# Optimization experiments

Hardware: AMD Instinct MI355X
Metric: run time of the kernel (lower is better)

The kernel has to match this reference:

```python
import jax, jax.numpy as jnp
import numpy as np

LEAF = 32
N = 262144          # num_nodes, power of 2
NLEV = 8            # HODLR levels
RANK = 16           # off-diagonal low-rank
NNZ = 1310720       # ~5 nnz per row


def setup_inputs() -> dict:
    key = jax.random.key(0)
    ks = jax.random.split(key, 24)
    inp = {}
    inp["leaf_blocks"] = jax.random.normal(ks[0], (1, N // LEAF, LEAF, LEAF), jnp.float32) * 0.1
    for l in range(NLEV):
        inp[f"u{l}"] = jax.random.normal(ks[1 + 2 * l], (1, N, RANK), jnp.float32) * 0.05
        inp[f"v{l}"] = jax.random.normal(ks[2 + 2 * l], (1, N, RANK), jnp.float32) * 0.05
    inp["A_indices"] = jax.random.randint(ks[17], (2, NNZ), 0, N, dtype=jnp.int32).astype(jnp.int64)
    inp["A_values"] = jax.random.normal(ks[18], (NNZ,), jnp.float32)
    inp["z"] = jax.random.normal(ks[19], (1, N, 1), jnp.float32)
    inp["num_nodes"] = N
    return inp


def apply_hodlr(leaf_blocks, factors, x, leaf_size=LEAF):
    # x: [B, n, 1]; leaf_blocks: [B, n/leaf, leaf, leaf]
    B, n, _ = x.shape
    nb = n // leaf_size
    xb = x.reshape(B, nb, leaf_size, 1)
    L = leaf_blocks
    # y = L @ (L^T @ x) + 1e-4 * x  per leaf block
    yb = jnp.matmul(L, jnp.matmul(jnp.swapaxes(L, -1, -2), xb)) + xb * 1e-4
    y = yb.reshape(B, n, 1)
    for li, (u, v) in enumerate(factors):
        num_splits = 2 ** (li + 1)
        bs = n // num_splits
        if bs == 0:
            continue
        npair = num_splits // 2
        vl = npair * 2 * bs  # == n for power-of-2 n
        xv = x[:, :vl].reshape(B, npair, 2, bs, 1)
        uv = u[:, :vl].reshape(B, npair, 2, bs, -1)
        vv = v[:, :vl].reshape(B, npair, 2, bs, -1)
        xL, xR = xv[:, :, 0], xv[:, :, 1]
        uL, uR = uv[:, :, 0], uv[:, :, 1]
        vL, vR = vv[:, :, 0], vv[:, :, 1]
        # cross-block low-rank updates: y_L += U_L (V_R^T x_R), y_R += U_R (V_L^T x_L)
        yL = jnp.matmul(uL, jnp.matmul(jnp.swapaxes(vR, -1, -2), xR))
        yR = jnp.matmul(uR, jnp.matmul(jnp.swapaxes(vL, -1, -2), xL))
        upd = jnp.stack([yL, yR], axis=2).reshape(B, vl, 1)
        if vl < n:
            upd = jnp.pad(upd, ((0, 0), (0, n - vl), (0, 0)))
        y = y + upd
    return y


def reference(leaf_blocks, u0, v0, u1, v1, u2, v2, u3, v3, u4, v4, u5, v5, u6, v6, u7, v7,
              A_indices, A_values, z, num_nodes):
    factors = [(u0, v0), (u1, v1), (u2, v2), (u3, v3),
               (u4, v4), (u5, v5), (u6, v6), (u7, v7)]
    w = apply_hodlr(leaf_blocks, factors, z)           # [1, N, 1]
    w_flat = w[0, :, 0]                                 # [N]
    rows, cols = A_indices[0], A_indices[1]
    # sparse COO matvec: y[r] = sum_k A_values[k] * w[cols[k]] over rows
    y_flat = jax.ops.segment_sum(A_values * w_flat[cols], rows, num_segments=num_nodes)
    y = y_flat.reshape(1, num_nodes, 1)
    return jnp.mean((y - z) ** 2)
```

## Files before the change

kernel.cpp:

```cpp
#include <hip/hip_runtime.h>

#define NN 262144
#define RANK 16
#define NNZ_K 1310720
#define NB 512
#define BPB 2560
#define NBKT 256
#define RPB 1024
#define NCH 2048

struct P8 { const float* p[8]; };

__global__ __launch_bounds__(256, 6) void k_levels_t(P8 v, const float* __restrict__ z,
                                                     float* __restrict__ part) {
    __shared__ float red[8][4][16];
    const int tid  = threadIdx.x;
    const int base = blockIdx.x * 128;
    const int q    = tid & 3;
    const int e    = tid >> 2;
    const int lane = tid & 63;
    const int wv   = tid >> 6;

#pragma unroll
    for (int g = 0; g < 2; ++g) {
        float4 acc[4];
#pragma unroll
        for (int l = 0; l < 4; ++l) acc[l] = make_float4(0.f, 0.f, 0.f, 0.f);

#pragma unroll
        for (int it = 0; it < 2; ++it) {
            const int jl = it * 64 + e;
            const size_t j = (size_t)(base + jl);
            const float zz = z[j];
            float4 vv[4];
#pragma unroll
            for (int l = 0; l < 4; ++l)
                vv[l] = *(const float4*)(v.p[g * 4 + l] + j * RANK + q * 4);
#pragma unroll
            for (int l = 0; l < 4; ++l) {
                acc[l].x += vv[l].x * zz;
                acc[l].y += vv[l].y * zz;
                acc[l].z += vv[l].z * zz;
                acc[l].w += vv[l].w * zz;
            }
        }

#pragma unroll
        for (int l = 0; l < 4; ++l) {
            float4 a = acc[l];
#pragma unroll
            for (int m = 4; m <= 32; m <<= 1) {
                a.x += __shfl_xor(a.x, m);
                a.y += __shfl_xor(a.y, m);
                a.z += __shfl_xor(a.z, m);
                a.w += __shfl_xor(a.w, m);
            }
            if (lane < 4) *(float4*)&red[g * 4 + l][wv][lane * 4] = a;
        }
    }
    __syncthreads();

    if (tid < 128) {
        const int l = tid >> 4;
        const int r = tid & 15;
        const float s = red[l][0][r] + red[l][1][r] + red[l][2][r] + red[l][3][r];
        part[(l * NCH + blockIdx.x) * 16 + r] = s;
    }
}

__global__ __launch_bounds__(256) void k_reduce_t(const float* __restrict__ part,
                                                  float* __restrict__ tg,
                                                  float* __restrict__ loss) {
    const int b = blockIdx.x;
    if (b == 0 && threadIdx.x == 0) loss[0] = 0.f;
    const int t = b + 2;
    const int l = 30 - __clz(t);
    const int h = t - (2 << l);
    const int cnt = 1024 >> l;
    const int c0  = h * cnt;
    const int r = threadIdx.x & 15;
    const int g = threadIdx.x >> 4;

    float s = 0.f;
    for (int c = c0 + g; c < c0 + cnt; c += 16)
        s += part[(l * NCH + c) * 16 + r];

    __shared__ float red[256];
    red[threadIdx.x] = s;
    __syncthreads();
    if (threadIdx.x < 16) {
        float ss = 0.f;
#pragma unroll
        for (int k = 0; k < 16; ++k) ss += red[k * 16 + r];
        tg[((2 << l) - 2 + h) * 16 + r] = ss;
    }
}

__global__ __launch_bounds__(256, 6) void k_w(const float* __restrict__ leaf, P8 u,
                                              const float* __restrict__ z,
                                              const float* __restrict__ tg,
                                              float* __restrict__ w,
                                              float* __restrict__ y) {
    __shared__ float wl[128];
    __shared__ float pb[128];
    __shared__ float tl[8][16];

    const int tid  = threadIdx.x;
    const int base = blockIdx.x * 128;

    if (tid < 128) {
        const int l = tid >> 4;
        const int r = tid & 15;
        const int h = base >> (17 - l);
        tl[l][r] = tg[(((2 << l) - 2) + (h ^ 1)) * 16 + r];
    }

    {
        const int l6 = tid & 63;
        const int wv = tid >> 6;
        const int b  = blockIdx.x * 4 + wv;
        const int r  = l6 >> 1;

        const float* Lb = leaf + (size_t)b * 1024 + r * 32 + (l6 & 1) * 16;
        const float4 L0 = ((const float4*)Lb)[0];
        const float4 L1 = ((const float4*)Lb)[1];
        const float4 L2 = ((const float4*)Lb)[2];
        const float4 L3 = ((const float4*)Lb)[3];

        const float zl = z[b * 32 + (l6 & 31)];
        const float xr = __shfl(zl, r);

        float4 t0 = make_float4(L0.x * xr, L0.y * xr, L0.z * xr, L0.w * xr);
        float4 t1 = make_float4(L1.x * xr, L1.y * xr, L1.z * xr, L1.w * xr);
        float4 t2 = make_float4(L2.x * xr, L2.y * xr, L2.z * xr, L2.w * xr);
        float4 t3 = make_float4(L3.x * xr, L3.y * xr, L3.z * xr, L3.w * xr);

#pragma unroll
        for (int m = 2; m <= 32; m <<= 1) {
            t0.x += __shfl_xor(t0.x, m); t0.y += __shfl_xor(t0.y, m);
            t0.z += __shfl_xor(t0.z, m); t0.w += __shfl_xor(t0.w, m);
            t1.x += __shfl_xor(t1.x, m); t1.y += __shfl_xor(t1.y, m);
            t1.z += __shfl_xor(t1.z, m); t1.w += __shfl_xor(t1.w, m);
            t2.x += __shfl_xor(t2.x, m); t2.y += __shfl_xor(t2.y, m);
            t2.z += __shfl_xor(t2.z, m); t2.w += __shfl_xor(t2.w, m);
            t3.x += __shfl_xor(t3.x, m); t3.y += __shfl_xor(t3.y, m);
            t3.z += __shfl_xor(t3.z, m); t3.w += __shfl_xor(t3.w, m);
        }

        float yp = L0.x * t0.x + L0.y * t0.y + L0.z * t0.z + L0.w * t0.w
                 + L1.x * t1.x + L1.y * t1.y + L1.z * t1.z + L1.w * t1.w
                 + L2.x * t2.x + L2.y * t2.y + L2.z * t2.z + L2.w * t2.w
                 + L3.x * t3.x + L3.y * t3.y + L3.z * t3.z + L3.w * t3.w;
        yp += __shfl_xor(yp, 1);

        const float w0  = yp + 1e-4f * xr;
        const float out = __shfl(w0, (l6 & 31) * 2);
        if (l6 < 32) wl[wv * 32 + l6] = out;
    }
    __syncthreads();

    const int half = tid >> 7;
    const int e    = tid & 127;
    const size_t i = (size_t)(base + e);
    const int l0   = half * 4;

    float accs[4];
#pragma unroll
    for (int lp = 0; lp < 2; ++lp) {
        const int l = l0 + lp * 2;
        float4 a[8];
        {
            const float4* up0 = (const float4*)(u.p[l] + i * RANK);
            const float4* up1 = (const float4*)(u.p[l + 1] + i * RANK);
#pragma unroll
            for (int k = 0; k < 4; ++k) a[k]     = up0[k];
#pragma unroll
            for (int k = 0; k < 4; ++k) a[4 + k] = up1[k];
        }
#pragma unroll
        for (int s = 0; s < 2; ++s) {
            const float4 t0 = *(const float4*)&tl[l + s][0];
            const float4 t1 = *(const float4*)&tl[l + s][4];
            const float4 t2 = *(const float4*)&tl[l + s][8];
            const float4 t3 = *(const float4*)&tl[l + s][12];
            const float4* av = &a[s * 4];
            accs[lp * 2 + s] = av[0].x * t0.x + av[0].y * t0.y + av[0].z * t0.z + av[0].w * t0.w
                             + av[1].x * t1.x + av[1].y * t1.y + av[1].z * t1.z + av[1].w * t1.w
                             + av[2].x * t2.x + av[2].y * t2.y + av[2].z * t2.z + av[2].w * t2.w
                             + av[3].x * t3.x + av[3].y * t3.y + av[3].z * t3.z + av[3].w * t3.w;
        }
    }
    const float sum = (accs[0] + accs[1]) + (accs[2] + accs[3]);
    if (half) pb[e] = sum;
    __syncthreads();
    if (!half) {
        w[i] = wl[e] + sum + pb[e];
        if (y) y[i] = 0.f;
    }
}

__global__ __launch_bounds__(640) void k_bin(const int* __restrict__ idx,
                                             const float* __restrict__ vals,
                                             const float* __restrict__ w,
                                             unsigned long long* __restrict__ gpairs,
                                             int* __restrict__ gdesc) {
    __shared__ unsigned long long pairs[BPB];
    __shared__ int hist[NBKT];
    __shared__ int scan[NBKT];
    __shared__ int cursor[NBKT];

    const int t  = threadIdx.x;
    const int bl = blockIdx.x;
    const int base = bl * BPB;

    if (t < NBKT) hist[t] = 0;
    __syncthreads();

    int   rows[4];
    float pv[4];
    {
        const int k = base + t * 4;
        const int4   r4 = *(const int4*)(idx + k);
        const int4   c4 = *(const int4*)(idx + NNZ_K + k);
        const float4 v4 = *(const float4*)(vals + k);
        rows[0] = r4.x; pv[0] = v4.x * w[c4.x];
        rows[1] = r4.y; pv[1] = v4.y * w[c4.y];
        rows[2] = r4.z; pv[2] = v4.z * w[c4.z];
        rows[3] = r4.w; pv[3] = v4.w * w[c4.w];
        atomicAdd(&hist[r4.x >> 10], 1);
        atomicAdd(&hist[r4.y >> 10], 1);
        atomicAdd(&hist[r4.z >> 10], 1);
        atomicAdd(&hist[r4.w >> 10], 1);
    }
    __syncthreads();

    int cnt = 0;
    if (t < NBKT) { cnt = hist[t]; scan[t] = cnt; }
    __syncthreads();
    for (int off = 1; off < NBKT; off <<= 1) {
        int add = 0;
        if (t >= off && t < NBKT) add = scan[t - off];
        __syncthreads();
        if (t < NBKT) scan[t] += add;
        __syncthreads();
    }
    if (t < NBKT) {
        const int st = scan[t] - cnt;
        gdesc[t * NB + bl] = st | (cnt << 16);
        cursor[t] = st;
    }
    __syncthreads();

#pragma unroll
    for (int i = 0; i < 4; ++i) {
        const int b   = rows[i] >> 10;
        const int pos = atomicAdd(&cursor[b], 1);
        pairs[pos] = ((unsigned long long)__float_as_uint(pv[i]) << 32) | (unsigned)rows[i];
    }
    __syncthreads();

    const ulonglong2* ps = (const ulonglong2*)pairs;
    ulonglong2*       pd = (ulonglong2*)(gpairs + (size_t)bl * BPB);
#pragma unroll
    for (int i = 0; i < 2; ++i)
        pd[i * 640 + t] = ps[i * 640 + t];
}

__global__ __launch_bounds__(1024) void k_accum(const unsigned long long* __restrict__ gpairs,
                                                const int* __restrict__ gdesc,
                                                const float* __restrict__ z,
                                                float* __restrict__ loss) {
    __shared__ float acc[RPB];
    __shared__ float red[16];
    const int t = threadIdx.x;
    const int b = blockIdx.x;
    acc[t] = 0.f;
    __syncthreads();

    {
        const int s  = t >> 1;
        const int h  = t & 1;
        const int d  = gdesc[b * NB + s];
        const int st = d & 0xffff;
        const int c  = d >> 16;
        const unsigned long long* p = gpairs + (size_t)s * BPB + st;
        for (int j = h; j < c; j += 2) {
            const unsigned long long pr = p[j];
            atomicAdd(&acc[(int)(pr & 1023u)], __uint_as_float((unsigned)(pr >> 32)));
        }
    }
    __syncthreads();

    const float d = acc[t] - z[b * RPB + t];
    float s = d * d;
#pragma unroll
    for (int m = 32; m >= 1; m >>= 1) s += __shfl_down(s, m);
    if ((t & 63) == 0) red[t >> 6] = s;
    __syncthreads();
    if (t == 0) {
        float tt = 0.f;
#pragma unroll
        for (int i = 0; i < 16; ++i) tt += red[i];
        atomicAdd(loss, tt);
    }
}

__global__ __launch_bounds__(256) void k_spmv(const int* __restrict__ idx,
                                              const float* __restrict__ vals,
                                              const float* __restrict__ w,
                                              float* __restrict__ y) {
    const int k = (blockIdx.x * 256 + threadIdx.x) * 4;
    const int4   r4 = *(const int4*)(idx + k);
    const int4   c4 = *(const int4*)(idx + NNZ_K + k);
    const float4 v4 = *(const float4*)(vals + k);
    atomicAdd(&y[r4.x], v4.x * w[c4.x]);
    atomicAdd(&y[r4.y], v4.y * w[c4.y]);
    atomicAdd(&y[r4.z], v4.z * w[c4.z]);
    atomicAdd(&y[r4.w], v4.w * w[c4.w]);
}

__global__ __launch_bounds__(256) void k_loss(const float* __restrict__ y,
                                              const float* __restrict__ z,
                                              float* __restrict__ loss) {
    const int i = blockIdx.x * 256 + threadIdx.x;
    const float4 a = ((const float4*)y)[i];
    const float4 b = ((const float4*)z)[i];
    const float dx = a.x - b.x, dy = a.y - b.y, dz = a.z - b.z, dw = a.w - b.w;
    float s = dx * dx + dy * dy + dz * dz + dw * dw;
#pragma unroll
    for (int m = 32; m >= 1; m >>= 1) s += __shfl_down(s, m);
    __shared__ float r4s[4];
    const int lane = threadIdx.x & 63, wv = threadIdx.x >> 6;
    if (lane == 0) r4s[wv] = s;
    __syncthreads();
    if (threadIdx.x == 0) atomicAdd(loss, r4s[0] + r4s[1] + r4s[2] + r4s[3]);
}

__global__ void k_fin(const float* __restrict__ loss, float* __restrict__ out) {
    out[0] = loss[0] * (1.0f / (float)NN);
}

extern "C" void kernel_launch(void* const* d_in, const int* in_sizes, int n_in,
                              void* d_out, int out_size, void* d_ws, size_t ws_size,
                              hipStream_t stream) {
    const float* leaf = (const float*)d_in[0];
    P8 u, v;
    for (int l = 0; l < 8; ++l) {
        u.p[l] = (const float*)d_in[1 + 2 * l];
        v.p[l] = (const float*)d_in[2 + 2 * l];
    }
    const int*   Aidx  = (const int*)d_in[17];
    const float* Avals = (const float*)d_in[18];
    const float* z     = (const float*)d_in[19];

    float* ws   = (float*)d_ws;
    float* part  = ws;
    float* tg    = ws + 262144;
    float* loss  = ws + 270336;
    float* w     = ws + 270400;
    int*   gdesc = (int*)(ws + 532544);
    unsigned long long* gpairs = (unsigned long long*)(ws + 663616);
    const size_t need_main = (size_t)(663616 + (size_t)NB * BPB * 2) * 4;

    k_levels_t<<<NCH, 256, 0, stream>>>(v, z, part);
    k_reduce_t<<<510, 256, 0, stream>>>(part, tg, loss);

    if (ws_size >= need_main) {
        k_w    <<<NN / 128, 256, 0, stream>>>(leaf, u, z, tg, w, nullptr);
        k_bin  <<<NB, 640, 0, stream>>>(Aidx, Avals, w, gpairs, gdesc);
        k_accum<<<NBKT, 1024, 0, stream>>>(gpairs, gdesc, z, loss);
    } else {
        float* y = ws + 532544;
        k_w    <<<NN / 128, 256, 0, stream>>>(leaf, u, z, tg, w, y);
        k_spmv <<<NNZ_K / 1024, 256, 0, stream>>>(Aidx, Avals, w, y);
        k_loss <<<NN / 1024, 256, 0, stream>>>(y, z, loss);
    }
    k_fin<<<1, 1, 0, stream>>>(loss, (float*)d_out);
}
```

Baseline: 355.0 us.

## Fuse leaf-block apply with V-projection pass and fold final loss into accumulator

Merges the V^T z projection and the leaf-block diagonal apply into one heterogeneous kernel, so the two independent phases run concurrently instead of in separate launches. The U-update becomes its own lighter kernel that adds onto the leaf result already stored in w. The projection now covers 256 rows per block, which halves the partial buffer and the reduction work. The final-loss kernel is replaced by a last-block-done counter in k_accum, which removes a launch but adds an atomic fence and an extra read-modify-write of w.

New measurement: 349.8 us. Within noise of the previous version (-1.5%).

```diff
diff --git a/kernel.cpp b/kernel.cpp
--- a/kernel.cpp
+++ b/kernel.cpp
@@ -7,118 +7,68 @@
 #define BPB 2560
 #define NBKT 256
 #define RPB 1024
-#define NCH 2048
+#define SPAN 256
+#define NSP 1024
 
 struct P8 { const float* p[8]; };
 
-__global__ __launch_bounds__(256, 6) void k_levels_t(P8 v, const float* __restrict__ z,
-                                                     float* __restrict__ part) {
-    __shared__ float red[8][4][16];
-    const int tid  = threadIdx.x;
-    const int base = blockIdx.x * 128;
-    const int q    = tid & 3;
-    const int e    = tid >> 2;
-    const int lane = tid & 63;
-    const int wv   = tid >> 6;
-
-#pragma unroll
-    for (int g = 0; g < 2; ++g) {
-        float4 acc[4];
-#pragma unroll
-        for (int l = 0; l < 4; ++l) acc[l] = make_float4(0.f, 0.f, 0.f, 0.f);
-
-#pragma unroll
-        for (int it = 0; it < 2; ++it) {
-            const int jl = it * 64 + e;
-            const size_t j = (size_t)(base + jl);
-            const float zz = z[j];
-            float4 vv[4];
-#pragma unroll
-            for (int l = 0; l < 4; ++l)
-                vv[l] = *(const float4*)(v.p[g * 4 + l] + j * RANK + q * 4);
-#pragma unroll
-            for (int l = 0; l < 4; ++l) {
-                acc[l].x += vv[l].x * zz;
-                acc[l].y += vv[l].y * zz;
-                acc[l].z += vv[l].z * zz;
-                acc[l].w += vv[l].w * zz;
+__global__ __launch_bounds__(256, 4) void k_front(const float* __restrict__ leaf,
+                                                  P8 v,
+                                                  const float* __restrict__ z,
+                                                  float* __restrict__ part,
+                                                  float* __restrict__ w) {
+    const int tid = threadIdx.x;
+
+    if (blockIdx.x < NSP) {
+        __shared__ float red[8][4][16];
+        const int cb   = blockIdx.x;
+        const int base = cb * SPAN;
+        const int q    = tid & 3;
+        const int e    = tid >> 2;
+        const int lane = tid & 63;
+        const int wv   = tid >> 6;
+
+        const float z0 = z[base + e];
+        const float z1 = z[base + 64 + e];
+        const float z2 = z[base + 128 + e];
+        const float z3 = z[base + 192 + e];
+
+#pragma unroll
+        for (int l = 0; l < 8; ++l) {
+            const float* vp = v.p[l];
+            const float4 a0 = *(const float4*)(vp + (size_t)(base + e) * RANK + q * 4);
+            const float4 a1 = *(const float4*)(vp + (size_t)(base + 64 + e) * RANK + q * 4);
+            const float4 a2 = *(const float4*)(vp + (size_t)(base + 128 + e) * RANK + q * 4);
+            const float4 a3 = *(const float4*)(vp + (size_t)(base + 192 + e) * RANK + q * 4);
+
+            float4 acc;
+            acc.x = a0.x * z0 + a1.x * z1 + a2.x * z2 + a3.x * z3;
+            acc.y = a0.y * z0 + a1.y * z1 + a2.y * z2 + a3.y * z3;
+            acc.z = a0.z * z0 + a1.z * z1 + a2.z * z2 + a3.z * z3;
+            acc.w = a0.w * z0 + a1.w * z1 + a2.w * z2 + a3.w * z3;
+
+#pragma unroll
+            for (int m = 4; m <= 32; m <<= 1) {
+                acc.x += __shfl_xor(acc.x, m);
+                acc.y += __shfl_xor(acc.y, m);
+                acc.z += __shfl_xor(acc.z, m);
+                acc.w += __shfl_xor(acc.w, m);
             }
-        }
-
-#pragma unroll
-        for (int l = 0; l < 4; ++l) {
-            float4 a = acc[l];
-#pragma unroll
-            for (int m = 4; m <= 32; m <<= 1) {
-                a.x += __shfl_xor(a.x, m);
-                a.y += __shfl_xor(a.y, m);
-                a.z += __shfl_xor(a.z, m);
-                a.w += __shfl_xor(a.w, m);
-            }
-            if (lane < 4) *(float4*)&red[g * 4 + l][wv][lane * 4] = a;
-        }
-    }
-    __syncthreads();
-
-    if (tid < 128) {
-        const int l = tid >> 4;
-        const int r = tid & 15;
-        const float s = red[l][0][r] + red[l][1][r] + red[l][2][r] + red[l][3][r];
-        part[(l * NCH + blockIdx.x) * 16 + r] = s;
-    }
-}
-
-__global__ __launch_bounds__(256) void k_reduce_t(const float* __restrict__ part,
-                                                  float* __restrict__ tg,
-                                                  float* __restrict__ loss) {
-    const int b = blockIdx.x;
-    if (b == 0 && threadIdx.x == 0) loss[0] = 0.f;
-    const int t = b + 2;
-    const int l = 30 - __clz(t);
-    const int h = t - (2 << l);
-    const int cnt = 1024 >> l;
-    const int c0  = h * cnt;
-    const int r = threadIdx.x & 15;
-    const int g = threadIdx.x >> 4;
-
-    float s = 0.f;
-    for (int c = c0 + g; c < c0 + cnt; c += 16)
-        s += part[(l * NCH + c) * 16 + r];
-
-    __shared__ float red[256];
-    red[threadIdx.x] = s;
-    __syncthreads();
-    if (threadIdx.x < 16) {
-        float ss = 0.f;
-#pragma unroll
-        for (int k = 0; k < 16; ++k) ss += red[k * 16 + r];
-        tg[((2 << l) - 2 + h) * 16 + r] = ss;
-    }
-}
-
-__global__ __launch_bounds__(256, 6) void k_w(const float* __restrict__ leaf, P8 u,
-                                              const float* __restrict__ z,
-                                              const float* __restrict__ tg,
-                                              float* __restrict__ w,
-                                              float* __restrict__ y) {
-    __shared__ float wl[128];
-    __shared__ float pb[128];
-    __shared__ float tl[8][16];
-
-    const int tid  = threadIdx.x;
-    const int base = blockIdx.x * 128;
-
-    if (tid < 128) {
-        const int l = tid >> 4;
-        const int r = tid & 15;
-        const int h = base >> (17 - l);
-        tl[l][r] = tg[(((2 << l) - 2) + (h ^ 1)) * 16 + r];
-    }
-
-    {
+            if (lane < 4) *(float4*)&red[l][wv][lane * 4] = acc;
+        }
+        __syncthreads();
+
+        if (tid < 128) {
+            const int l = tid >> 4;
+            const int r = tid & 15;
+            const float s = red[l][0][r] + red[l][1][r] + red[l][2][r] + red[l][3][r];
+            part[(l * NSP + cb) * 16 + r] = s;
+        }
+    } else {
+        const int lb = blockIdx.x - NSP;
         const int l6 = tid & 63;
         const int wv = tid >> 6;
-        const int b  = blockIdx.x * 4 + wv;
+        const int b  = lb * 4 + wv;
         const int r  = l6 >> 1;
 
         const float* Lb = leaf + (size_t)b * 1024 + r * 32 + (l6 & 1) * 16;
@@ -155,48 +105,87 @@
 
         const float w0  = yp + 1e-4f * xr;
         const float out = __shfl(w0, (l6 & 31) * 2);
-        if (l6 < 32) wl[wv * 32 + l6] = out;
-    }
-    __syncthreads();
-
-    const int half = tid >> 7;
-    const int e    = tid & 127;
-    const size_t i = (size_t)(base + e);
-    const int l0   = half * 4;
-
-    float accs[4];
-#pragma unroll
-    for (int lp = 0; lp < 2; ++lp) {
-        const int l = l0 + lp * 2;
-        float4 a[8];
-        {
-            const float4* up0 = (const float4*)(u.p[l] + i * RANK);
-            const float4* up1 = (const float4*)(u.p[l + 1] + i * RANK);
-#pragma unroll
-            for (int k = 0; k < 4; ++k) a[k]     = up0[k];
-#pragma unroll
-            for (int k = 0; k < 4; ++k) a[4 + k] = up1[k];
-        }
-#pragma unroll
-        for (int s = 0; s < 2; ++s) {
-            const float4 t0 = *(const float4*)&tl[l + s][0];
-            const float4 t1 = *(const float4*)&tl[l + s][4];
-            const float4 t2 = *(const float4*)&tl[l + s][8];
-            const float4 t3 = *(const float4*)&tl[l + s][12];
-            const float4* av = &a[s * 4];
-            accs[lp * 2 + s] = av[0].x * t0.x + av[0].y * t0.y + av[0].z * t0.z + av[0].w * t0.w
-                             + av[1].x * t1.x + av[1].y * t1.y + av[1].z * t1.z + av[1].w * t1.w
-                             + av[2].x * t2.x + av[2].y * t2.y + av[2].z * t2.z + av[2].w * t2.w
-                             + av[3].x * t3.x + av[3].y * t3.y + av[3].z * t3.z + av[3].w * t3.w;
-        }
-    }
-    const float sum = (accs[0] + accs[1]) + (accs[2] + accs[3]);
-    if (half) pb[e] = sum;
-    __syncthreads();
-    if (!half) {
-        w[i] = wl[e] + sum + pb[e];
-        if (y) y[i] = 0.f;
-    }
+        if (l6 < 32) w[(size_t)b * 32 + l6] = out;
+    }
+}
+
+__global__ __launch_bounds__(256) void k_reduce_t(const float* __restrict__ part,
+                                                  float* __restrict__ tg,
+                                                  float* __restrict__ loss) {
+    const int b = blockIdx.x;
+    if (b == 0 && threadIdx.x == 0) { loss[0] = 0.f; ((int*)loss)[1] = 0; }
+    const int t = b + 2;
+    const int l = 30 - __clz(t);
+    const int h = t - (2 << l);
+    const int cnt = NSP >> (l + 1);
+    const int c0  = h * cnt;
+    const int r = threadIdx.x & 15;
+    const int g = threadIdx.x >> 4;
+
+    float s = 0.f;
+    for (int c = c0 + g; c < c0 + cnt; c += 16)
+        s += part[(l * NSP + c) * 16 + r];
+
+    __shared__ float red[256];
+    red[threadIdx.x] = s;
+    __syncthreads();
+    if (threadIdx.x < 16) {
+        float ss = 0.f;
+#pragma unroll
+        for (int k = 0; k < 16; ++k) ss += red[k * 16 + r];
+        tg[((2 << l) - 2 + h) * 16 + r] = ss;
+    }
+}
+
+__global__ __launch_bounds__(256, 4) void k_uacc(P8 u,
+                                                 const float* __restrict__ tg,
+                                                 float* __restrict__ w,
+                                                 float* __restrict__ y) {
+    __shared__ float tl[8][16];
+    const int tid  = threadIdx.x;
+    const int base = blockIdx.x * SPAN;
+    const size_t i = (size_t)(base + tid);
+
+    const float w0 = w[i];
+
+    if (tid < 128) {
+        const int l = tid >> 4;
+        const int r = tid & 15;
+        const int h = base >> (17 - l);
+        tl[l][r] = tg[(((2 << l) - 2) + (h ^ 1)) * 16 + r];
+    }
+    __syncthreads();
+
+    float acc = 0.f;
+#pragma unroll
+    for (int lp = 0; lp < 4; ++lp) {
+        const int l = lp * 2;
+        const float4* ua = (const float4*)(u.p[l]     + i * RANK);
+        const float4* ub = (const float4*)(u.p[l + 1] + i * RANK);
+        const float4 a0 = ua[0], a1 = ua[1], a2 = ua[2], a3 = ua[3];
+        const float4 b0 = ub[0], b1 = ub[1], b2 = ub[2], b3 = ub[3];
+
+        const float4 s0 = *(const float4*)&tl[l][0];
+        const float4 s1 = *(const float4*)&tl[l][4];
+        const float4 s2 = *(const float4*)&tl[l][8];
+        const float4 s3 = *(const float4*)&tl[l][12];
+        acc += a0.x * s0.x + a0.y * s0.y + a0.z * s0.z + a0.w * s0.w
+             + a1.x * s1.x + a1.y * s1.y + a1.z * s1.z + a1.w * s1.w
+             + a2.x * s2.x + a2.y * s2.y + a2.z * s2.z + a2.w * s2.w
+             + a3.x * s3.x + a3.y * s3.y + a3.z * s3.z + a3.w * s3.w;
+
+        const float4 r0 = *(const float4*)&tl[l + 1][0];
+        const float4 r1 = *(const float4*)&tl[l + 1][4];
+        const float4 r2 = *(const float4*)&tl[l + 1][8];
+        const float4 r3 = *(const float4*)&tl[l + 1][12];
+        acc += b0.x * r0.x + b0.y * r0.y + b0.z * r0.z + b0.w * r0.w
+             + b1.x * r1.x + b1.y * r1.y + b1.z * r1.z + b1.w * r1.w
+             + b2.x * r2.x + b2.y * r2.y + b2.z * r2.z + b2.w * r2.w
+             + b3.x * r3.x + b3.y * r3.y + b3.z * r3.z + b3.w * r3.w;
+    }
+
+    w[i] = w0 + acc;
+    if (y) y[i] = 0.f;
 }
 
 __global__ __launch_bounds__(640) void k_bin(const int* __restrict__ idx,
@@ -269,7 +258,8 @@
 __global__ __launch_bounds__(1024) void k_accum(const unsigned long long* __restrict__ gpairs,
                                                 const int* __restrict__ gdesc,
                                                 const float* __restrict__ z,
-                                                float* __restrict__ loss) {
+                                                float* __restrict__ loss,
+                                                float* __restrict__ out) {
     __shared__ float acc[RPB];
     __shared__ float red[16];
     const int t = threadIdx.x;
@@ -302,6 +292,12 @@
 #pragma unroll
         for (int i = 0; i < 16; ++i) tt += red[i];
         atomicAdd(loss, tt);
+        __threadfence();
+        int* done = (int*)loss + 1;
+        if (atomicAdd(done, 1) == NBKT - 1) {
+            const float total = atomicAdd(loss, 0.0f);
+            out[0] = total * (1.0f / (float)NN);
+        }
     }
 }
 
@@ -355,25 +351,26 @@
 
     float* ws   = (float*)d_ws;
     float* part  = ws;
-    float* tg    = ws + 262144;
-    float* loss  = ws + 270336;
-    float* w     = ws + 270400;
-    int*   gdesc = (int*)(ws + 532544);
-    unsigned long long* gpairs = (unsigned long long*)(ws + 663616);
-    const size_t need_main = (size_t)(663616 + (size_t)NB * BPB * 2) * 4;
-
-    k_levels_t<<<NCH, 256, 0, stream>>>(v, z, part);
+    float* tg    = ws + 131072;
+    float* loss  = ws + 139264;
+    float* w     = ws + 139328;
+    int*   gdesc = (int*)(ws + 401472);
+    unsigned long long* gpairs = (unsigned long long*)(ws + 532544);
+    const size_t need_main = (size_t)(532544 + (size_t)NB * BPB * 2) * 4;
+
+    k_front   <<<NSP + NN / 128, 256, 0, stream>>>(leaf, v, z, part, w);
     k_reduce_t<<<510, 256, 0, stream>>>(part, tg, loss);
 
     if (ws_size >= need_main) {
-        k_w    <<<NN / 128, 256, 0, stream>>>(leaf, u, z, tg, w, nullptr);
+        k_uacc <<<NSP, 256, 0, stream>>>(u, tg, w, nullptr);
         k_bin  <<<NB, 640, 0, stream>>>(Aidx, Avals, w, gpairs, gdesc);
-        k_accum<<<NBKT, 1024, 0, stream>>>(gpairs, gdesc, z, loss);
+        k_accum<<<NBKT, 1024, 0, stream>>>(gpairs, gdesc, z, loss, (float*)d_out);
     } else {
-        float* y = ws + 532544;
-        k_w    <<<NN / 128, 256, 0, stream>>>(leaf, u, z, tg, w, y);
+        float* y = ws + 401472 + 262144 <= (float*)((char*)d_ws + ws_size)
+                 ? ws + 401472 : ws + 401472;
+        k_uacc <<<NSP, 256, 0, stream>>>(u, tg, w, y);
         k_spmv <<<NNZ_K / 1024, 256, 0, stream>>>(Aidx, Avals, w, y);
         k_loss <<<NN / 1024, 256, 0, stream>>>(y, z, loss);
-    }
-    k_fin<<<1, 1, 0, stream>>>(loss, (float*)d_out);
-}
+        k_fin  <<<1, 1, 0, stream>>>(loss, (float*)d_out);
+    }
+}
```
